# Kernel tuning notes

Measured on AMD Instinct MI355X. Metric: run time of the kernel, lower is better.

The kernel has to match this reference:

```python
import jax, jax.numpy as jnp
import numpy as np


def setup_inputs() -> dict:
    key = jax.random.key(0)
    k1, k2, k3, k4 = jax.random.split(key, 4)
    B, K, M, X, Y = 64, 4, 3, 256, 256
    predictions = jax.random.uniform(k1, (B, K, X, Y), dtype=jnp.float32)
    inputs = jax.random.normal(k2, (B, M, X, Y), dtype=jnp.float32)
    heart = jax.random.randint(k3, (B, 1, X, Y), 0, 2, dtype=jnp.int32)
    mu_data = jax.random.normal(k4, (K, M), dtype=jnp.float32)
    return {"predictions": predictions, "inputs": inputs, "heart": heart, "mu_data": mu_data}


def reference(predictions, inputs, heart, mu_data):
    eps = 1e-10
    # Boolean-mask gather is equivalent to multiplying by the 0/1 mask, since
    # everything downstream is a sum over the masked positions.
    mask = (heart[:, 0] == 1).astype(predictions.dtype)          # [B, X, Y]
    pm = predictions * mask[:, None]                             # [B, K, X, Y]
    num = jnp.einsum('bkxy,bmxy->bkm', pm, inputs)               # weighted sums
    den = jnp.sum(pm, axis=(2, 3)) + eps                         # [B, K]
    mu_mean = jnp.mean(num / den[..., None], axis=0)             # [K, M]
    return jnp.sum((mu_data - mu_mean) ** 2)
```

## Files before the change

kernel.cpp:

```cpp
#include <hip/hip_runtime.h>

#define B_    64
#define K_    4
#define M_    3
#define NPIX  65536
#define CHUNKS 64
#define TPB   256
#define NV    16

__global__ __launch_bounds__(TPB) void partial_kernel(
    const float* __restrict__ pred,
    const float* __restrict__ inp,
    const int*   __restrict__ heart,
    float* __restrict__ num_ws,
    float* __restrict__ den_ws)
{
    const int b     = blockIdx.x >> 6;
    const int chunk = blockIdx.x & 63;
    const int pix   = chunk * (NPIX / CHUNKS) + (int)threadIdx.x * 4;

    const int4 h = *reinterpret_cast<const int4*>(heart + (size_t)b * NPIX + pix);
    float4 mask;
    mask.x = (h.x == 1) ? 1.0f : 0.0f;
    mask.y = (h.y == 1) ? 1.0f : 0.0f;
    mask.z = (h.z == 1) ? 1.0f : 0.0f;
    mask.w = (h.w == 1) ? 1.0f : 0.0f;

    float4 in[M_];
#pragma unroll
    for (int m = 0; m < M_; ++m)
        in[m] = *reinterpret_cast<const float4*>(inp + ((size_t)b * M_ + m) * NPIX + pix);

    float val[NV];
#pragma unroll
    for (int k = 0; k < K_; ++k) {
        float4 p = *reinterpret_cast<const float4*>(pred + ((size_t)b * K_ + k) * NPIX + pix);
        float4 pm;
        pm.x = p.x * mask.x; pm.y = p.y * mask.y;
        pm.z = p.z * mask.z; pm.w = p.w * mask.w;
        val[k] = (pm.x + pm.y) + (pm.z + pm.w);
#pragma unroll
        for (int m = 0; m < M_; ++m)
            val[4 + k * M_ + m] = pm.x * in[m].x + pm.y * in[m].y
                                + pm.z * in[m].z + pm.w * in[m].w;
    }

#pragma unroll
    for (int off = 32; off > 0; off >>= 1) {
#pragma unroll
        for (int i = 0; i < NV; ++i)
            val[i] += __shfl_down(val[i], off, 64);
    }

    __shared__ float smem[TPB / 64][NV];
    const int lane = threadIdx.x & 63;
    const int wave = threadIdx.x >> 6;
    if (lane == 0) {
#pragma unroll
        for (int i = 0; i < NV; ++i) smem[wave][i] = val[i];
    }
    __syncthreads();

    if (threadIdx.x < NV) {
        float s = smem[0][threadIdx.x] + smem[1][threadIdx.x]
                + smem[2][threadIdx.x] + smem[3][threadIdx.x];
        if (threadIdx.x < K_)
            atomicAdd(&den_ws[b * K_ + threadIdx.x], s);
        else
            atomicAdd(&num_ws[b * (K_ * M_) + (threadIdx.x - K_)], s);
    }
}

__global__ __launch_bounds__(64) void finalize_kernel(
    const float* __restrict__ num_ws,
    const float* __restrict__ den_ws,
    const float* __restrict__ mu_data,
    float* __restrict__ out)
{
    const int b = threadIdx.x;
    float r[K_ * M_];
#pragma unroll
    for (int k = 0; k < K_; ++k) {
        const float den = den_ws[b * K_ + k] + 1e-10f;
        const float inv = 1.0f / den;
#pragma unroll
        for (int m = 0; m < M_; ++m)
            r[k * M_ + m] = num_ws[b * (K_ * M_) + k * M_ + m] * inv;
    }
#pragma unroll
    for (int off = 32; off > 0; off >>= 1) {
#pragma unroll
        for (int i = 0; i < K_ * M_; ++i)
            r[i] += __shfl_down(r[i], off, 64);
    }
    if (b == 0) {
        float s = 0.0f;
#pragma unroll
        for (int i = 0; i < K_ * M_; ++i) {
            const float d = mu_data[i] - r[i] * (1.0f / (float)B_);
            s += d * d;
        }
        out[0] = s;
    }
}

extern "C" void kernel_launch(void* const* d_in, const int* in_sizes, int n_in,
                              void* d_out, int out_size, void* d_ws, size_t ws_size,
                              hipStream_t stream) {
    const float* pred    = (const float*)d_in[0];
    const float* inp     = (const float*)d_in[1];
    const int*   heart   = (const int*)d_in[2];
    const float* mu_data = (const float*)d_in[3];
    float* out = (float*)d_out;

    float* num_ws = (float*)d_ws;
    float* den_ws = num_ws + B_ * K_ * M_;

    hipMemsetAsync(d_ws, 0, (size_t)(B_ * K_ * M_ + B_ * K_) * sizeof(float), stream);

    partial_kernel<<<B_ * CHUNKS, TPB, 0, stream>>>(pred, inp, heart, num_ws, den_ws);
    finalize_kernel<<<1, 64, 0, stream>>>(num_ws, den_ws, mu_data, out);
}
```

Before: 151.9 us.

## Fuse finalize into partial kernel via last-block ticket and halve grid

```diff
diff --git a/kernel.cpp b/kernel.cpp
--- a/kernel.cpp
+++ b/kernel.cpp
@@ -1,106 +1,129 @@
 #include <hip/hip_runtime.h>
 
-#define B_    64
-#define K_    4
-#define M_    3
-#define NPIX  65536
-#define CHUNKS 64
-#define TPB   256
-#define NV    16
+#define B_     64
+#define K_     4
+#define M_     3
+#define NPIX   65536
+#define CHUNKS 32
+#define GRID_  (B_ * CHUNKS)
+#define TPB    256
+#define ITERS  2
+#define NV     16
+#define KM     (K_ * M_)
 
-__global__ __launch_bounds__(TPB) void partial_kernel(
+__global__ __launch_bounds__(TPB) void fused_kernel(
     const float* __restrict__ pred,
     const float* __restrict__ inp,
     const int*   __restrict__ heart,
+    const float* __restrict__ mu_data,
     float* __restrict__ num_ws,
-    float* __restrict__ den_ws)
+    float* __restrict__ den_ws,
+    unsigned int* __restrict__ counter,
+    float* __restrict__ out)
 {
-    const int b     = blockIdx.x >> 6;
-    const int chunk = blockIdx.x & 63;
-    const int pix   = chunk * (NPIX / CHUNKS) + (int)threadIdx.x * 4;
-
-    const int4 h = *reinterpret_cast<const int4*>(heart + (size_t)b * NPIX + pix);
-    float4 mask;
-    mask.x = (h.x == 1) ? 1.0f : 0.0f;
-    mask.y = (h.y == 1) ? 1.0f : 0.0f;
-    mask.z = (h.z == 1) ? 1.0f : 0.0f;
-    mask.w = (h.w == 1) ? 1.0f : 0.0f;
-
-    float4 in[M_];
-#pragma unroll
-    for (int m = 0; m < M_; ++m)
-        in[m] = *reinterpret_cast<const float4*>(inp + ((size_t)b * M_ + m) * NPIX + pix);
+    const int b     = blockIdx.x >> 5;
+    const int chunk = blockIdx.x & (CHUNKS - 1);
 
     float val[NV];
 #pragma unroll
-    for (int k = 0; k < K_; ++k) {
-        float4 p = *reinterpret_cast<const float4*>(pred + ((size_t)b * K_ + k) * NPIX + pix);
-        float4 pm;
-        pm.x = p.x * mask.x; pm.y = p.y * mask.y;
-        pm.z = p.z * mask.z; pm.w = p.w * mask.w;
-        val[k] = (pm.x + pm.y) + (pm.z + pm.w);
+    for (int i = 0; i < NV; ++i) val[i] = 0.0f;
+
+#pragma unroll
+    for (int it = 0; it < ITERS; ++it) {
+        const int pix = chunk * (NPIX / CHUNKS) + it * (TPB * 4) + (int)threadIdx.x * 4;
+
+        const int4 h = *reinterpret_cast<const int4*>(heart + (size_t)b * NPIX + pix);
+        float4 mask;
+        mask.x = (h.x == 1) ? 1.0f : 0.0f;
+        mask.y = (h.y == 1) ? 1.0f : 0.0f;
+        mask.z = (h.z == 1) ? 1.0f : 0.0f;
+        mask.w = (h.w == 1) ? 1.0f : 0.0f;
+
+        float4 in[M_];
 #pragma unroll
         for (int m = 0; m < M_; ++m)
-            val[4 + k * M_ + m] = pm.x * in[m].x + pm.y * in[m].y
-                                + pm.z * in[m].z + pm.w * in[m].w;
+            in[m] = *reinterpret_cast<const float4*>(inp + ((size_t)b * M_ + m) * NPIX + pix);
+
+#pragma unroll
+        for (int k = 0; k < K_; ++k) {
+            float4 p = *reinterpret_cast<const float4*>(pred + ((size_t)b * K_ + k) * NPIX + pix);
+            float4 pm;
+            pm.x = p.x * mask.x; pm.y = p.y * mask.y;
+            pm.z = p.z * mask.z; pm.w = p.w * mask.w;
+            val[k] += (pm.x + pm.y) + (pm.z + pm.w);
+#pragma unroll
+            for (int m = 0; m < M_; ++m)
+                val[4 + k * M_ + m] += pm.x * in[m].x + pm.y * in[m].y
+                                     + pm.z * in[m].z + pm.w * in[m].w;
+        }
     }
 
 #pragma unroll
-    for (int off = 32; off > 0; off >>= 1) {
+    for (int off = 32; off >= 4; off >>= 1) {
 #pragma unroll
         for (int i = 0; i < NV; ++i)
             val[i] += __shfl_down(val[i], off, 64);
     }
 
-    __shared__ float smem[TPB / 64][NV];
+    __shared__ float smem[TPB / 64][4][NV];
     const int lane = threadIdx.x & 63;
     const int wave = threadIdx.x >> 6;
-    if (lane == 0) {
+    if (lane < 4) {
 #pragma unroll
-        for (int i = 0; i < NV; ++i) smem[wave][i] = val[i];
+        for (int i = 0; i < NV; ++i) smem[wave][lane][i] = val[i];
     }
     __syncthreads();
 
     if (threadIdx.x < NV) {
-        float s = smem[0][threadIdx.x] + smem[1][threadIdx.x]
-                + smem[2][threadIdx.x] + smem[3][threadIdx.x];
+        float s = 0.0f;
+#pragma unroll
+        for (int w = 0; w < TPB / 64; ++w)
+#pragma unroll
+            for (int l = 0; l < 4; ++l)
+                s += smem[w][l][threadIdx.x];
         if (threadIdx.x < K_)
             atomicAdd(&den_ws[b * K_ + threadIdx.x], s);
         else
-            atomicAdd(&num_ws[b * (K_ * M_) + (threadIdx.x - K_)], s);
+            atomicAdd(&num_ws[b * KM + (threadIdx.x - K_)], s);
     }
-}
 
-__global__ __launch_bounds__(64) void finalize_kernel(
-    const float* __restrict__ num_ws,
-    const float* __restrict__ den_ws,
-    const float* __restrict__ mu_data,
-    float* __restrict__ out)
-{
-    const int b = threadIdx.x;
-    float r[K_ * M_];
+    __shared__ unsigned int ticket;
+    __threadfence();
+    __syncthreads();
+    if (threadIdx.x == 0)
+        ticket = atomicAdd(counter, 1u);
+    __syncthreads();
+    if (ticket != GRID_ - 1) return;
+
+    if (threadIdx.x < B_) {
+        __threadfence();
+        const int bb = threadIdx.x;
+        float r[KM];
 #pragma unroll
-    for (int k = 0; k < K_; ++k) {
-        const float den = den_ws[b * K_ + k] + 1e-10f;
-        const float inv = 1.0f / den;
+        for (int k = 0; k < K_; ++k) {
+            const float den = __hip_atomic_load(&den_ws[bb * K_ + k],
+                                __ATOMIC_RELAXED, __HIP_MEMORY_SCOPE_AGENT) + 1e-10f;
+            const float inv = 1.0f / den;
 #pragma unroll
-        for (int m = 0; m < M_; ++m)
-            r[k * M_ + m] = num_ws[b * (K_ * M_) + k * M_ + m] * inv;
-    }
+            for (int m = 0; m < M_; ++m)
+                r[k * M_ + m] = __hip_atomic_load(&num_ws[bb * KM + k * M_ + m],
+                                  __ATOMIC_RELAXED, __HIP_MEMORY_SCOPE_AGENT) * inv;
+        }
 #pragma unroll
-    for (int off = 32; off > 0; off >>= 1) {
+        for (int off = 32; off > 0; off >>= 1) {
 #pragma unroll
-        for (int i = 0; i < K_ * M_; ++i)
-            r[i] += __shfl_down(r[i], off, 64);
-    }
-    if (b == 0) {
-        float s = 0.0f;
+            for (int i = 0; i < KM; ++i)
+                r[i] += __shfl_down(r[i], off, 64);
+        }
+        if (bb == 0) {
+            float s = 0.0f;
 #pragma unroll
-        for (int i = 0; i < K_ * M_; ++i) {
-            const float d = mu_data[i] - r[i] * (1.0f / (float)B_);
-            s += d * d;
+            for (int i = 0; i < KM; ++i) {
+                const float d = mu_data[i] - r[i] * (1.0f / (float)B_);
+                s += d * d;
+            }
+            out[0] = s;
         }
-        out[0] = s;
     }
 }
 
@@ -114,10 +137,11 @@
     float* out = (float*)d_out;
 
     float* num_ws = (float*)d_ws;
-    float* den_ws = num_ws + B_ * K_ * M_;
+    float* den_ws = num_ws + B_ * KM;
+    unsigned int* counter = (unsigned int*)(den_ws + B_ * K_);
 
-    hipMemsetAsync(d_ws, 0, (size_t)(B_ * K_ * M_ + B_ * K_) * sizeof(float), stream);
+    hipMemsetAsync(d_ws, 0, (size_t)(B_ * KM + B_ * K_ + 1) * sizeof(float), stream);
 
-    partial_kernel<<<B_ * CHUNKS, TPB, 0, stream>>>(pred, inp, heart, num_ws, den_ws);
-    finalize_kernel<<<1, 64, 0, stream>>>(num_ws, den_ws, mu_data, out);
+    fused_kernel<<<GRID_, TPB, 0, stream>>>(pred, inp, heart, mu_data,
+                                            num_ws, den_ws, counter, out);
 }
```

Result: slower. 466.7 us (+207.3%).
